# Kernel optimization log

Hardware: AMD Instinct MI355X
Metric: run time of the kernel (lower is better)

Reference implementation:

```python
import jax, jax.numpy as jnp
import numpy as np

NUM_HEADS = 16
WINDOW = 128

def setup_inputs() -> dict:
    key = jax.random.key(0)
    ks = jax.random.split(key, 9)
    E, B, S = 1024, 2, 2048
    sc = 1.0 / np.sqrt(E)
    return {
        'x':  jax.random.normal(ks[0], (B, S, E), jnp.float32),
        'Wq': jax.random.normal(ks[1], (E, E), jnp.float32) * sc,
        'bq': jax.random.normal(ks[2], (E,), jnp.float32) * 0.02,
        'Wk': jax.random.normal(ks[3], (E, E), jnp.float32) * sc,
        'bk': jax.random.normal(ks[4], (E,), jnp.float32) * 0.02,
        'Wv': jax.random.normal(ks[5], (E, E), jnp.float32) * sc,
        'bv': jax.random.normal(ks[6], (E,), jnp.float32) * 0.02,
        'Wo': jax.random.normal(ks[7], (E, E), jnp.float32) * sc,
        'bo': jax.random.normal(ks[8], (E,), jnp.float32) * 0.02,
    }

def reference(x, Wq, bq, Wk, bk, Wv, bv, Wo, bo):
    B, S, E = x.shape
    H = NUM_HEADS
    D = E // H
    # projections -> [B, H, S, D]
    q = (x @ Wq + bq).reshape(B, S, H, D).transpose(0, 2, 1, 3)
    k = (x @ Wk + bk).reshape(B, S, H, D).transpose(0, 2, 1, 3)
    v = (x @ Wv + bv).reshape(B, S, H, D).transpose(0, 2, 1, 3)
    # dense scores [B, H, S, S]
    energy = jnp.einsum('bhqd,bhkd->bhqk', q, k)
    idx = jnp.arange(S)
    blocked = jnp.abs(idx[:, None] - idx[None, :]) > WINDOW  # True = outside band
    neg = jnp.finfo(jnp.float32).min
    energy = jnp.where(blocked[None, None], neg, energy)
    # note: original scales by sqrt(emb_size), not sqrt(head_dim)
    att = jax.nn.softmax(energy / jnp.sqrt(jnp.float32(E)), axis=-1)
    out = jnp.einsum('bhqk,bhkd->bhqd', att, v)
    out = out.transpose(0, 2, 1, 3).reshape(B, S, E)
    return out @ Wo + bo
```

## Files before the change

### kernel.cpp

```cpp
#include <hip/hip_runtime.h>

typedef unsigned short u16;
typedef unsigned int u32;
typedef __attribute__((ext_vector_type(8))) short bf16x8;
typedef __attribute__((ext_vector_type(4))) float f32x4;
typedef __attribute__((ext_vector_type(4))) unsigned int u32x4;
typedef __attribute__((ext_vector_type(4))) unsigned short u16x4;

#define DEV static __device__ __forceinline__

DEV u16 f2bf(float f) {
  unsigned u = __builtin_bit_cast(unsigned, f);
  u += 0x7FFFu + ((u >> 16) & 1u);
  return (u16)(u >> 16);
}

DEV u32 cvt_pk_bf16(float lo, float hi) {
  u32 d;
  asm("v_cvt_pk_bf16_f32 %0, %1, %2" : "=v"(d) : "v"(lo), "v"(hi));
  return d;
}

DEV void load_lds16(const void* g, void* l) {
  __builtin_amdgcn_global_load_lds(
      (const __attribute__((address_space(1))) unsigned int*)g,
      (__attribute__((address_space(3))) unsigned int*)l, 16, 0, 0);
}


__global__ void k_prep(const float* __restrict__ x,
                       const float* __restrict__ bq, const float* __restrict__ bk,
                       const float* __restrict__ bv,
                       const float* __restrict__ Wq, const float* __restrict__ Wk,
                       const float* __restrict__ Wv, const float* __restrict__ Wo,
                       u16* __restrict__ xb, u16* __restrict__ wtqkv,
                       u16* __restrict__ wto, float* __restrict__ bias) {
  const int tid = threadIdx.x;
  const int bid = blockIdx.x;
  if (bid < 4096) {
    __shared__ float t[32][33];
    const int wi = bid >> 10, inner = bid & 1023;
    const float* W = (wi == 0) ? Wq : (wi == 1) ? Wk : (wi == 2) ? Wv : Wo;
    u16* Wt = (wi == 3) ? wto : wtqkv + (size_t)wi * 1024 * 1024;
    const int tx = tid & 31, ty = tid >> 5;
    const int c0 = (inner & 31) * 32, r0 = (inner >> 5) * 32;
#pragma unroll
    for (int i = 0; i < 4; ++i)
      t[ty + i * 8][tx] = W[(size_t)(r0 + ty + i * 8) * 1024 + c0 + tx];
    __syncthreads();
#pragma unroll
    for (int i = 0; i < 4; ++i)
      Wt[(size_t)(c0 + ty + i * 8) * 1024 + r0 + tx] = f2bf(t[tx][ty + i * 8]);
  } else if (bid < 8192) {
    int i = ((bid - 4096) * 256 + tid) * 4;
    f32x4 v = *(const f32x4*)(x + i);
    u16x4 o;
#pragma unroll
    for (int j = 0; j < 4; ++j) o[j] = f2bf(v[j]);
    *(u16x4*)(xb + i) = o;
  } else {
    int i = (bid - 8192) * 256 + tid;
    float v = (i < 1024) ? bq[i] : (i < 2048) ? bk[i - 1024] : bv[i - 2048];
    bias[i] = v;
  }
}


template <int BN, typename CT>
__launch_bounds__(256) __global__
void k_gemm_bt(const u16* __restrict__ A, const u16* __restrict__ Bt,
               const float* __restrict__ bias, CT* __restrict__ C, int ldc,
               u16* __restrict__ vtp) {
  constexpr int BM = 128, BK = 64;
  constexpr int NJ = BN / 32;
  constexpr int EPW = BN / 2 + 4;
  __shared__ __align__(16) char smem[(BM + BN) * BK * 2];
  u16* lA = (u16*)smem;
  u16* lB = (u16*)(smem + BM * BK * 2);
  float (*ep)[16][EPW] = (float (*)[16][EPW])smem;

  const int tid = threadIdx.x;
  const int w = tid >> 6, lane = tid & 63, g = lane >> 4, n16 = lane & 15;
  const int wm = w >> 1, wn = w & 1;
  const int m0 = blockIdx.y * BM, n0 = blockIdx.x * BN;

  f32x4 acc[4][NJ] = {};
  for (int t = 0; t < 16; ++t) {
    if (t) __syncthreads();
    const int k0 = t * 64;
#pragma unroll
    for (int r = 0; r < BM / 32; ++r) {
      int s = r * 256 + tid;
      int row = s >> 3, cc = (s & 7) ^ (row & 7);
      load_lds16(A + (size_t)(m0 + row) * 1024 + k0 + cc * 8, lA + s * 8);
    }
#pragma unroll
    for (int r = 0; r < BN / 32; ++r) {
      int s = r * 256 + tid;
      int row = s >> 3, cc = (s & 7) ^ (row & 7);
      load_lds16(Bt + (size_t)(n0 + row) * 1024 + k0 + cc * 8, lB + s * 8);
    }
    __syncthreads();
#pragma unroll
    for (int kh = 0; kh < 2; ++kh) {
      const int csel = ((kh * 4 + g) ^ (n16 & 7)) * 8;
      bf16x8 af[4], bfr[NJ];
#pragma unroll
      for (int i = 0; i < 4; ++i)
        af[i] = *(const bf16x8*)&lA[(wm * 64 + i * 16 + n16) * 64 + csel];
#pragma unroll
      for (int j = 0; j < NJ; ++j)
        bfr[j] = *(const bf16x8*)&lB[(wn * (BN / 2) + j * 16 + n16) * 64 + csel];
      __builtin_amdgcn_s_setprio(1);
#pragma unroll
      for (int i = 0; i < 4; ++i)
#pragma unroll
        for (int j = 0; j < NJ; ++j)
          acc[i][j] = __builtin_amdgcn_mfma_f32_16x16x32_bf16(af[i], bfr[j], acc[i][j], 0, 0, 0);
      __builtin_amdgcn_s_setprio(0);
    }
  }
  __syncthreads();

  const int m_base = m0 + wm * 64, n_base = n0 + wn * (BN / 2);
  bool vmode = false;
  if constexpr (sizeof(CT) == 2 && BN == 128)
    vmode = (vtp != nullptr) && (n_base >= 2048);

#pragma unroll
  for (int i = 0; i < 4; ++i) {
#pragma unroll
    for (int j = 0; j < NJ; ++j) {
      float bv = bias[n_base + j * 16 + n16];
#pragma unroll
      for (int jj = 0; jj < 4; ++jj)
        ep[w][g * 4 + jj][j * 16 + n16] = acc[i][j][jj] + bv;
    }
    asm volatile("s_waitcnt lgkmcnt(0)" ::: "memory");
    if (vmode) {
      const int head = (n_base - 2048) >> 6;
      const int m_row0 = m_base + i * 16;
      const int bb = m_row0 >> 11, s0 = m_row0 & 2047;
      union { u16 a[16]; u32x4 v[2]; } pk;
#pragma unroll
      for (int r = 0; r < 16; ++r) pk.a[r] = f2bf(ep[w][r][lane]);
      size_t vrow = ((size_t)(bb * 16 + head) * 64 + lane) * 2048 + s0;
      *(u32x4*)(vtp + vrow) = pk.v[0];
      *(u32x4*)(vtp + vrow + 8) = pk.v[1];
    } else {
      constexpr int CPR = BN / 8;
      constexpr int P = 16 * CPR / 64;
#pragma unroll
      for (int p = 0; p < P; ++p) {
        int fl = p * 64 + lane;
        int row = fl / CPR, cc = (fl % CPR) * 4;
        f32x4 v = *(const f32x4*)&ep[w][row][cc];
        size_t off = (size_t)(m_base + i * 16 + row) * ldc + n_base + cc;
        if constexpr (sizeof(CT) == 2) {
          u16x4 o;
#pragma unroll
          for (int q = 0; q < 4; ++q) o[q] = f2bf(v[q]);
          *(u16x4*)(C + off) = o;
        } else {
          *(f32x4*)(C + off) = v;
        }
      }
    }
    asm volatile("s_waitcnt lgkmcnt(0)" ::: "memory");
  }
}


__launch_bounds__(256, 3) __global__
void k_attn(const u16* __restrict__ qkv, const u16* __restrict__ vt,
            u16* __restrict__ attn) {
  __shared__ __align__(16) u16 KV[20480];
  __shared__ __align__(16) u16 Ostg[4][16][64];
  const int tid = threadIdx.x;
  const int w = tid >> 6, lane = tid & 63, g = lane >> 4, n16 = lane & 15;
  const int bid = (blockIdx.x & 7) * 128 + (blockIdx.x >> 3);
  const int qt = bid & 31, h = (bid >> 5) & 15, b = bid >> 9;
  const int q0b = qt * 64;
  const int kvb = q0b - 128;
  const int q0 = q0b + w * 16;
  const int kv0 = q0 - 128;
  const int q = q0 + n16;
  const int bh = b * 16 + h;

  {
    const u16* kpart = qkv + (size_t)b * 2048 * 3072 + 1024 + h * 64;
#pragma unroll
    for (int i = 0; i < 10; ++i) {
      int c = i * 256 + tid;
      int r = c >> 3, cc = c & 7;
      int srcr = min(max(kvb + r, 0), 2047);
      load_lds16(kpart + (size_t)srcr * 3072 + (cc ^ (r & 7)) * 8, &KV[c * 8]);
    }
  }

  const size_t rowQ = (size_t)(b * 2048 + q) * 3072 + h * 64;
  bf16x8 qf0 = *(const bf16x8*)(qkv + rowQ + g * 8);
  bf16x8 qf1 = *(const bf16x8*)(qkv + rowQ + 32 + g * 8);
  __syncthreads();

  const int kbase = 8 * (n16 >> 2) + (n16 & 3);
  const int wrel = 16 * w;
  f32x4 sv[18];
#pragma unroll
  for (int t = 0; t < 18; ++t) {
    int kr = wrel + 32 * (t >> 1) + 4 * (t & 1) + kbase;
    int krl = min(kr, 319);
    int p = krl & 7;
    const u16* kp = &KV[krl * 64];
    bf16x8 kf0 = *(const bf16x8*)(kp + (g ^ p) * 8);
    bf16x8 kf1 = *(const bf16x8*)(kp + ((g + 4) ^ p) * 8);
    f32x4 s = {0.f, 0.f, 0.f, 0.f};
    s = __builtin_amdgcn_mfma_f32_16x16x32_bf16(kf0, qf0, s, 0, 0, 0);
    s = __builtin_amdgcn_mfma_f32_16x16x32_bf16(kf1, qf1, s, 0, 0, 0);
    sv[t] = s;
  }
  __syncthreads();

  {
    const u16* vpart = vt + (size_t)bh * 64 * 2048;
#pragma unroll
    for (int i = 0; i < 10; ++i) {
      int c = i * 256 + tid;
      int d = c / 40, cc = c - d * 40;
      int j = cc ^ (d & 7);
      int srck = min(max(kvb + j * 8, 0), 2040);
      load_lds16(vpart + (size_t)d * 2048 + srck, &KV[c * 8]);
    }
  }

  const float NEG = -__builtin_inff();
#pragma unroll
  for (int t = 0; t < 18; ++t) {
    int kb = kv0 + 32 * (t >> 1) + 4 * (t & 1) + 8 * g;
#pragma unroll
    for (int jj = 0; jj < 4; ++jj) {
      int k = kb + jj;
      bool ok = ((unsigned)k < 2048u) && ((unsigned)(q - k + 128) <= 256u);
      sv[t][jj] = ok ? sv[t][jj] : NEG;
    }
  }

  float mx = NEG;
#pragma unroll
  for (int t = 0; t < 18; ++t)
    mx = fmaxf(mx, fmaxf(fmaxf(sv[t][0], sv[t][1]), fmaxf(sv[t][2], sv[t][3])));
  mx = fmaxf(mx, __shfl_xor(mx, 16));
  mx = fmaxf(mx, __shfl_xor(mx, 32));

  const float c = 0.04508422017f;
  const float nmc = -mx * c;
  float sum = 0.f;
#pragma unroll
  for (int t = 0; t < 18; ++t)
#pragma unroll
    for (int jj = 0; jj < 4; ++jj) {
      float p = exp2f(fmaf(sv[t][jj], c, nmc));
      sv[t][jj] = p;
      sum += p;
    }
  sum += __shfl_xor(sum, 16);
  sum += __shfl_xor(sum, 32);
  const float inv = 1.f / sum;

  __syncthreads();

  f32x4 oacc[4] = {};
#pragma unroll
  for (int s = 0; s < 9; ++s) {
    union { u32 u[4]; bf16x8 v; } paf;
    paf.u[0] = cvt_pk_bf16(sv[2 * s][0], sv[2 * s][1]);
    paf.u[1] = cvt_pk_bf16(sv[2 * s][2], sv[2 * s][3]);
    paf.u[2] = cvt_pk_bf16(sv[2 * s + 1][0], sv[2 * s + 1][1]);
    paf.u[3] = cvt_pk_bf16(sv[2 * s + 1][2], sv[2 * s + 1][3]);
    int jc = min(2 * w + 4 * s + g, 39);
#pragma unroll
    for (int dt = 0; dt < 4; ++dt) {
      int d = dt * 16 + n16;
      bf16x8 vf = *(const bf16x8*)&KV[d * 320 + (jc ^ (d & 7)) * 8];
      oacc[dt] = __builtin_amdgcn_mfma_f32_16x16x32_bf16(paf.v, vf, oacc[dt], 0, 0, 0);
    }
  }

  float rs[4];
#pragma unroll
  for (int jj = 0; jj < 4; ++jj) rs[jj] = __shfl(inv, 4 * g + jj);

#pragma unroll
  for (int dt = 0; dt < 4; ++dt)
#pragma unroll
    for (int jj = 0; jj < 4; ++jj)
      Ostg[w][g * 4 + jj][dt * 16 + n16] = f2bf(oacc[dt][jj] * rs[jj]);
  asm volatile("s_waitcnt lgkmcnt(0)" ::: "memory");
#pragma unroll
  for (int p = 0; p < 2; ++p) {
    int fl = p * 512 + lane * 8;
    int row = fl >> 6, col = fl & 63;
    u32x4 v = *(const u32x4*)&Ostg[w][row][col];
    *(u32x4*)(attn + (size_t)(b * 2048 + q0 + row) * 1024 + h * 64 + col) = v;
  }
}


extern "C" void kernel_launch(void* const* d_in, const int* in_sizes, int n_in,
                              void* d_out, int out_size, void* d_ws, size_t ws_size,
                              hipStream_t stream) {
  const float* x  = (const float*)d_in[0];
  const float* Wq = (const float*)d_in[1];
  const float* bq = (const float*)d_in[2];
  const float* Wk = (const float*)d_in[3];
  const float* bk = (const float*)d_in[4];
  const float* Wv = (const float*)d_in[5];
  const float* bv = (const float*)d_in[6];
  const float* Wo = (const float*)d_in[7];
  const float* bo = (const float*)d_in[8];

  char* ws = (char*)d_ws;
  const size_t MB = 1ull << 20;
  u16*   xb    = (u16*)(ws + 0);
  u16*   wtqkv = (u16*)(ws + 8 * MB);
  u16*   wto   = (u16*)(ws + 14 * MB);
  float* bias  = (float*)(ws + 16 * MB);
  u16*   qkvb  = (u16*)(ws + 17 * MB);
  u16*   vtb   = (u16*)(ws + 41 * MB);
  u16*   attnb = (u16*)(ws + 0);

  k_prep<<<8204, 256, 0, stream>>>(x, bq, bk, bv, Wq, Wk, Wv, Wo,
                                   xb, wtqkv, wto, bias);
  k_gemm_bt<128, u16><<<dim3(24, 32), 256, 0, stream>>>(xb, wtqkv, bias, qkvb, 3072, vtb);
  k_attn<<<1024, 256, 0, stream>>>(qkvb, vtb, attnb);
  k_gemm_bt<64, float><<<dim3(16, 32), 256, 0, stream>>>(attnb, wto, bo, (float*)d_out,
                                                         1024, nullptr);
}
```

Before: 78.68 us.

## Prefetch next K tile into LDS during MFMA and swizzle block order

The GEMM loop now reads the whole K-tile's fragments into registers, syncs, issues the global-to-LDS loads for the next tile, and then runs the MFMAs. This lets the memory loads overlap the matrix math within a single LDS buffer. Block indices are remapped in a strided swizzle to improve L2 locality, and launch bounds request two blocks per CU. The cost is higher register pressure from holding both k-halves of fragments, plus an extra barrier per iteration.

```diff
diff --git a/kernel.cpp b/kernel.cpp
--- a/kernel.cpp
+++ b/kernel.cpp
@@ -67,7 +67,7 @@
 
 
 template <int BN, typename CT>
-__launch_bounds__(256) __global__
+__launch_bounds__(256, 2) __global__
 void k_gemm_bt(const u16* __restrict__ A, const u16* __restrict__ Bt,
                const float* __restrict__ bias, CT* __restrict__ C, int ldc,
                u16* __restrict__ vtp) {
@@ -82,44 +82,58 @@
   const int tid = threadIdx.x;
   const int w = tid >> 6, lane = tid & 63, g = lane >> 4, n16 = lane & 15;
   const int wm = w >> 1, wn = w & 1;
-  const int m0 = blockIdx.y * BM, n0 = blockIdx.x * BN;
+
+  const int nbx = gridDim.x;
+  const int flat = blockIdx.y * nbx + blockIdx.x;
+  const int cpx = (nbx * gridDim.y) >> 3;
+  const int swz = (flat & 7) * cpx + (flat >> 3);
+  const int m0 = (swz / nbx) * BM, n0 = (swz % nbx) * BN;
+
+#define STAGE(k0)                                                            \
+  do {                                                                       \
+    _Pragma("unroll")                                                        \
+    for (int r = 0; r < BM / 32; ++r) {                                      \
+      int s = r * 256 + tid;                                                 \
+      int row = s >> 3, cc = (s & 7) ^ (row & 7);                            \
+      load_lds16(A + (size_t)(m0 + row) * 1024 + (k0) + cc * 8, lA + s * 8); \
+    }                                                                        \
+    _Pragma("unroll")                                                        \
+    for (int r = 0; r < BN / 32; ++r) {                                      \
+      int s = r * 256 + tid;                                                 \
+      int row = s >> 3, cc = (s & 7) ^ (row & 7);                            \
+      load_lds16(Bt + (size_t)(n0 + row) * 1024 + (k0) + cc * 8, lB + s * 8);\
+    }                                                                        \
+  } while (0)
 
   f32x4 acc[4][NJ] = {};
+  STAGE(0);
   for (int t = 0; t < 16; ++t) {
-    if (t) __syncthreads();
-    const int k0 = t * 64;
-#pragma unroll
-    for (int r = 0; r < BM / 32; ++r) {
-      int s = r * 256 + tid;
-      int row = s >> 3, cc = (s & 7) ^ (row & 7);
-      load_lds16(A + (size_t)(m0 + row) * 1024 + k0 + cc * 8, lA + s * 8);
-    }
-#pragma unroll
-    for (int r = 0; r < BN / 32; ++r) {
-      int s = r * 256 + tid;
-      int row = s >> 3, cc = (s & 7) ^ (row & 7);
-      load_lds16(Bt + (size_t)(n0 + row) * 1024 + k0 + cc * 8, lB + s * 8);
-    }
     __syncthreads();
+    bf16x8 af[2][4], bfr[2][NJ];
 #pragma unroll
     for (int kh = 0; kh < 2; ++kh) {
       const int csel = ((kh * 4 + g) ^ (n16 & 7)) * 8;
-      bf16x8 af[4], bfr[NJ];
 #pragma unroll
       for (int i = 0; i < 4; ++i)
-        af[i] = *(const bf16x8*)&lA[(wm * 64 + i * 16 + n16) * 64 + csel];
+        af[kh][i] = *(const bf16x8*)&lA[(wm * 64 + i * 16 + n16) * 64 + csel];
 #pragma unroll
       for (int j = 0; j < NJ; ++j)
-        bfr[j] = *(const bf16x8*)&lB[(wn * (BN / 2) + j * 16 + n16) * 64 + csel];
-      __builtin_amdgcn_s_setprio(1);
+        bfr[kh][j] = *(const bf16x8*)&lB[(wn * (BN / 2) + j * 16 + n16) * 64 + csel];
+    }
+    __syncthreads();
+    if (t < 15) STAGE((t + 1) * 64);
+    __builtin_amdgcn_s_setprio(1);
+#pragma unroll
+    for (int kh = 0; kh < 2; ++kh)
 #pragma unroll
       for (int i = 0; i < 4; ++i)
 #pragma unroll
         for (int j = 0; j < NJ; ++j)
-          acc[i][j] = __builtin_amdgcn_mfma_f32_16x16x32_bf16(af[i], bfr[j], acc[i][j], 0, 0, 0);
-      __builtin_amdgcn_s_setprio(0);
-    }
-  }
+          acc[i][j] =
+              __builtin_amdgcn_mfma_f32_16x16x32_bf16(af[kh][i], bfr[kh][j], acc[i][j], 0, 0, 0);
+    __builtin_amdgcn_s_setprio(0);
+  }
+#undef STAGE
   __syncthreads();
 
   const int m_base = m0 + wm * 64, n_base = n0 + wn * (BN / 2);
```

Result: faster. 76.35 us (-3.0%).
